# Kernel optimization log

Hardware: AMD Instinct MI355X
Metric: run time of the kernel (lower is better)

## Reference

```python
import jax, jax.numpy as jnp
import numpy as np

ALPHA = 0.2  # LeakyReLU negative slope


def setup_inputs() -> dict:
    key = jax.random.key(0)
    k1, k2, k3, k4 = jax.random.split(key, 4)
    B, N, IN_F, OUT_F = 8, 2048, 128, 64
    inputs = jax.random.normal(k1, (B, N, IN_F), dtype=jnp.float32)
    nodes_embedding = jax.random.normal(k2, (B, N, OUT_F), dtype=jnp.float32)
    # xavier-uniform-like init (gain 1.414)
    limW = 1.414 * np.sqrt(6.0 / (IN_F + OUT_F))
    W = jax.random.uniform(k3, (IN_F, OUT_F), dtype=jnp.float32, minval=-limW, maxval=limW)
    lima = 1.414 * np.sqrt(6.0 / (4 * OUT_F + 1))
    a = jax.random.uniform(k4, (4 * OUT_F, 1), dtype=jnp.float32, minval=-lima, maxval=lima)
    return {"inputs": inputs, "nodes_embedding": nodes_embedding, "W": W, "a": a}


def reference(inputs, nodes_embedding, W, a):
    # x_w: [B,N,F]
    x_w = jnp.matmul(inputs, W)
    # h: [B,N,2F]
    h = jnp.concatenate([nodes_embedding, x_w], axis=2)
    twoF = h.shape[-1]
    # Separable form of concat-based attention: a_input[b,i,j] = [h_i, h_j],
    # so a_input @ a = (h_i . a1) + (h_j . a2). Avoids the O(B*N^2*4F) tensor.
    a1 = a[:twoF, 0]  # [2F]
    a2 = a[twoF:, 0]  # [2F]
    s1 = jnp.einsum('bnf,f->bn', h, a1)  # [B,N]
    s2 = jnp.einsum('bnf,f->bn', h, a2)  # [B,N]
    e = jax.nn.leaky_relu(s1[:, :, None] + s2[:, None, :], negative_slope=ALPHA)  # [B,N,N]
    attention = jax.nn.softmax(e, axis=2)  # softmax over j
    # dropout: eval mode (training=False) -> identity
    h_prime = jnp.matmul(attention, x_w)  # [B,N,F]
    return (jax.nn.relu(h_prime), attention)
```

## Files before the change

kernel.cpp:

```cpp
#include <hip/hip_runtime.h>

#define ALPHA 0.2f
#define B_    8
#define N_    2048
#define INF_  128
#define OUTF_ 64

typedef __attribute__((ext_vector_type(8))) short short8;
typedef __attribute__((ext_vector_type(4))) float f32x4;

__device__ __forceinline__ unsigned short f2bf(float f) {
    unsigned int x = __float_as_uint(f);
    return (unsigned short)((x + 0x7fffu + ((x >> 16) & 1u)) >> 16);
}

__global__ __launch_bounds__(256) void prep_kernel(
    const float* __restrict__ inp,
    const float* __restrict__ nodes,
    const float* __restrict__ Wm,
    const float* __restrict__ av,
    unsigned short* __restrict__ xwT,
    float* __restrict__ s1_out,
    float* __restrict__ s2_out)
{
    __shared__ float w_lds[INF_ * OUTF_];
    __shared__ float in_lds[16 * INF_];
    __shared__ __align__(16) unsigned short t_lds[64 * 16];
    const int tid  = threadIdx.x;
    const int wave = tid >> 6, lane = tid & 63;
    const int r0   = blockIdx.x * 16;

    {
        const float4* Wv = (const float4*)Wm;
        float4* wd = (float4*)w_lds;
        #pragma unroll
        for (int q = 0; q < 8; q++) wd[tid + q * 256] = Wv[tid + q * 256];
        const float4* Iv = (const float4*)(inp + (size_t)r0 * INF_);
        float4* id4 = (float4*)in_lds;
        id4[tid]       = Iv[tid];
        id4[tid + 256] = Iv[tid + 256];
    }
    __syncthreads();

    float acc[4] = {0.f, 0.f, 0.f, 0.f};
    const float* inw = &in_lds[(wave * 4) * INF_];
    #pragma unroll 4
    for (int k = 0; k < INF_; k++) {
        float wv = w_lds[k * OUTF_ + lane];
        acc[0] += inw[k]            * wv;
        acc[1] += inw[INF_ + k]     * wv;
        acc[2] += inw[2 * INF_ + k] * wv;
        acc[3] += inw[3 * INF_ + k] * wv;
    }

    const float a1n = av[lane];
    const float a1x = av[64 + lane];
    const float a2n = av[128 + lane];
    const float a2x = av[192 + lane];

    #pragma unroll
    for (int rr = 0; rr < 4; rr++) {
        const int row = r0 + wave * 4 + rr;
        float nf = nodes[(size_t)row * OUTF_ + lane];
        float p1 = nf * a1n + acc[rr] * a1x;
        float p2 = nf * a2n + acc[rr] * a2x;
        #pragma unroll
        for (int off = 32; off; off >>= 1) {
            p1 += __shfl_down(p1, off);
            p2 += __shfl_down(p2, off);
        }
        if (lane == 0) { s1_out[row] = p1; s2_out[row] = p2; }
        t_lds[lane * 16 + wave * 4 + rr] = f2bf(acc[rr]);
    }
    __syncthreads();

    {
        const int n  = tid >> 2, c0 = (tid & 3) * 4;
        const int b  = r0 >> 11, rb = r0 & (N_ - 1);
        *(uint2*)(xwT + ((size_t)b * OUTF_ + n) * N_ + rb + c0) =
            *(const uint2*)&t_lds[n * 16 + c0];
    }
}

__global__ __launch_bounds__(256) void attn_kernel(
    const unsigned short* __restrict__ xwT,
    const float* __restrict__ s1g,
    const float* __restrict__ s2g,
    float* __restrict__ out_h,
    float* __restrict__ out_att)
{
    __shared__ float s2_lds[N_];
    __shared__ float s1_lds[64];
    __shared__ float m_lds[64];
    __shared__ float li_lds[64];
    __shared__ float redmax[4];

    const int tid  = threadIdx.x;
    const int wave = tid >> 6, lane = tid & 63;
    const int b  = blockIdx.x >> 5;
    const int i0 = (blockIdx.x & 31) << 6;

    {
        const float4* s2v = (const float4*)(s2g + b * N_);
        float4* d4 = (float4*)s2_lds;
        d4[tid]       = s2v[tid];
        d4[tid + 256] = s2v[tid + 256];
    }
    if (tid < 64) s1_lds[tid] = s1g[b * N_ + i0 + tid];
    __syncthreads();

    {
        float lm = -1e30f;
        for (int idx = tid; idx < N_; idx += 256) lm = fmaxf(lm, s2_lds[idx]);
        #pragma unroll
        for (int off = 32; off; off >>= 1) lm = fmaxf(lm, __shfl_xor(lm, off));
        if (lane == 0) redmax[wave] = lm;
    }
    __syncthreads();
    const float s2max = fmaxf(fmaxf(redmax[0], redmax[1]),
                              fmaxf(redmax[2], redmax[3]));

    {
        const int i = tid >> 2, jo = tid & 3;
        const float s1v = s1_lds[i];
        const float vm = s1v + s2max;
        const float m = vm > 0.f ? vm : ALPHA * vm;
        float l = 0.f;
        for (int j4 = jo * 4; j4 < N_; j4 += 16) {
            float4 s = *(const float4*)&s2_lds[j4];
            float v0 = s1v + s.x, v1 = s1v + s.y, v2 = s1v + s.z, v3 = s1v + s.w;
            l += __expf(fmaxf(v0, ALPHA * v0) - m);
            l += __expf(fmaxf(v1, ALPHA * v1) - m);
            l += __expf(fmaxf(v2, ALPHA * v2) - m);
            l += __expf(fmaxf(v3, ALPHA * v3) - m);
        }
        l += __shfl_xor(l, 1);
        l += __shfl_xor(l, 2);
        if (jo == 0) { m_lds[i] = m; li_lds[i] = 1.f / l; }
    }
    __syncthreads();

    const int row16 = lane & 15;
    const int quad  = lane >> 4;
    const int irow  = wave * 16 + row16;
    const float s1v = s1_lds[irow];
    const float mr  = m_lds[irow];
    const float lir = li_lds[irow];

    const unsigned short* bptr[4];
    #pragma unroll
    for (int g = 0; g < 4; g++)
        bptr[g] = xwT + ((size_t)b * OUTF_ + g * 16 + row16) * N_ + quad * 8;

    float* attp = out_att + ((size_t)(b * N_ + i0 + irow)) * N_ + quad * 8;
    const float* s2q = s2_lds + quad * 8;

    f32x4 acc0 = {0.f,0.f,0.f,0.f}, acc1 = {0.f,0.f,0.f,0.f};
    f32x4 acc2 = {0.f,0.f,0.f,0.f}, acc3 = {0.f,0.f,0.f,0.f};

    uint4 bnext[4];
    #pragma unroll
    for (int g = 0; g < 4; g++) bnext[g] = *(const uint4*)bptr[g];

    for (int jt = 0; jt < N_; jt += 32) {
        uint4 bc0 = bnext[0], bc1 = bnext[1], bc2 = bnext[2], bc3 = bnext[3];
        const int jn = (jt + 32) & (N_ - 1);
        #pragma unroll
        for (int g = 0; g < 4; g++) bnext[g] = *(const uint4*)(bptr[g] + jn);

        float4 sa = *(const float4*)(s2q + jt);
        float4 sb = *(const float4*)(s2q + jt + 4);
        float av8[8];
        {
            float v;
            v = s1v + sa.x; av8[0] = __expf(fmaxf(v, ALPHA * v) - mr) * lir;
            v = s1v + sa.y; av8[1] = __expf(fmaxf(v, ALPHA * v) - mr) * lir;
            v = s1v + sa.z; av8[2] = __expf(fmaxf(v, ALPHA * v) - mr) * lir;
            v = s1v + sa.w; av8[3] = __expf(fmaxf(v, ALPHA * v) - mr) * lir;
            v = s1v + sb.x; av8[4] = __expf(fmaxf(v, ALPHA * v) - mr) * lir;
            v = s1v + sb.y; av8[5] = __expf(fmaxf(v, ALPHA * v) - mr) * lir;
            v = s1v + sb.z; av8[6] = __expf(fmaxf(v, ALPHA * v) - mr) * lir;
            v = s1v + sb.w; av8[7] = __expf(fmaxf(v, ALPHA * v) - mr) * lir;
        }
        *(float4*)(attp + jt)     = make_float4(av8[0], av8[1], av8[2], av8[3]);
        *(float4*)(attp + jt + 4) = make_float4(av8[4], av8[5], av8[6], av8[7]);

        short8 a8;
        #pragma unroll
        for (int jj = 0; jj < 8; jj++) a8[jj] = (short)f2bf(av8[jj]);

        acc0 = __builtin_amdgcn_mfma_f32_16x16x32_bf16(a8, *(short8*)&bc0, acc0, 0, 0, 0);
        acc1 = __builtin_amdgcn_mfma_f32_16x16x32_bf16(a8, *(short8*)&bc1, acc1, 0, 0, 0);
        acc2 = __builtin_amdgcn_mfma_f32_16x16x32_bf16(a8, *(short8*)&bc2, acc2, 0, 0, 0);
        acc3 = __builtin_amdgcn_mfma_f32_16x16x32_bf16(a8, *(short8*)&bc3, acc3, 0, 0, 0);
    }

    {
        const size_t hb = ((size_t)(b * N_) + i0 + wave * 16) * OUTF_;
        #pragma unroll
        for (int r = 0; r < 4; r++) {
            const size_t ro = hb + (size_t)(quad * 4 + r) * OUTF_ + row16;
            out_h[ro]      = fmaxf(acc0[r], 0.f);
            out_h[ro + 16] = fmaxf(acc1[r], 0.f);
            out_h[ro + 32] = fmaxf(acc2[r], 0.f);
            out_h[ro + 48] = fmaxf(acc3[r], 0.f);
        }
    }
}

extern "C" void kernel_launch(void* const* d_in, const int* in_sizes, int n_in,
                              void* d_out, int out_size, void* d_ws, size_t ws_size,
                              hipStream_t stream) {
    const float* inp   = (const float*)d_in[0];
    const float* nodes = (const float*)d_in[1];
    const float* Wm    = (const float*)d_in[2];
    const float* av    = (const float*)d_in[3];

    float* out_h   = (float*)d_out;
    float* out_att = out_h + (size_t)B_ * N_ * OUTF_;

    unsigned short* xwT = (unsigned short*)d_ws;
    float* s1_ws = (float*)((char*)d_ws + (size_t)B_ * OUTF_ * N_ * sizeof(unsigned short));
    float* s2_ws = s1_ws + (size_t)B_ * N_;

    prep_kernel<<<(B_ * N_) / 16, 256, 0, stream>>>(inp, nodes, Wm, av,
                                                    xwT, s1_ws, s2_ws);
    attn_kernel<<<(B_ * N_) / 64, 256, 0, stream>>>(xwT, s1_ws, s2_ws,
                                                    out_h, out_att);
}
```

Baseline: 193.1 us.

## Split attention kernel over key dimension with LDS cross-wave reduction

Result: no change. 193.8 us (+0.3%).

```diff
diff --git a/kernel.cpp b/kernel.cpp
--- a/kernel.cpp
+++ b/kernel.cpp
@@ -82,7 +82,7 @@
     }
 }
 
-__global__ __launch_bounds__(256) void attn_kernel(
+__global__ __launch_bounds__(256, 4) void attn_kernel(
     const unsigned short* __restrict__ xwT,
     const float* __restrict__ s1g,
     const float* __restrict__ s2g,
@@ -90,15 +90,16 @@
     float* __restrict__ out_att)
 {
     __shared__ float s2_lds[N_];
-    __shared__ float s1_lds[64];
-    __shared__ float m_lds[64];
-    __shared__ float li_lds[64];
+    __shared__ float s1_lds[16];
+    __shared__ float m_lds[16];
+    __shared__ float li_lds[16];
     __shared__ float redmax[4];
+    __shared__ __align__(16) float red_lds[4][16][68];
 
     const int tid  = threadIdx.x;
     const int wave = tid >> 6, lane = tid & 63;
-    const int b  = blockIdx.x >> 5;
-    const int i0 = (blockIdx.x & 31) << 6;
+    const int b   = blockIdx.x >> 7;
+    const int i0g = blockIdx.x * 16;
 
     {
         const float4* s2v = (const float4*)(s2g + b * N_);
@@ -106,7 +107,7 @@
         d4[tid]       = s2v[tid];
         d4[tid + 256] = s2v[tid + 256];
     }
-    if (tid < 64) s1_lds[tid] = s1g[b * N_ + i0 + tid];
+    if (tid < 16) s1_lds[tid] = s1g[i0g + tid];
     __syncthreads();
 
     {
@@ -121,12 +122,12 @@
                               fmaxf(redmax[2], redmax[3]));
 
     {
-        const int i = tid >> 2, jo = tid & 3;
+        const int i = tid >> 4, jo = tid & 15;
         const float s1v = s1_lds[i];
         const float vm = s1v + s2max;
         const float m = vm > 0.f ? vm : ALPHA * vm;
         float l = 0.f;
-        for (int j4 = jo * 4; j4 < N_; j4 += 16) {
+        for (int j4 = jo * 4; j4 < N_; j4 += 64) {
             float4 s = *(const float4*)&s2_lds[j4];
             float v0 = s1v + s.x, v1 = s1v + s.y, v2 = s1v + s.z, v3 = s1v + s.w;
             l += __expf(fmaxf(v0, ALPHA * v0) - m);
@@ -134,26 +135,26 @@
             l += __expf(fmaxf(v2, ALPHA * v2) - m);
             l += __expf(fmaxf(v3, ALPHA * v3) - m);
         }
-        l += __shfl_xor(l, 1);
-        l += __shfl_xor(l, 2);
+        #pragma unroll
+        for (int off = 8; off; off >>= 1) l += __shfl_xor(l, off);
         if (jo == 0) { m_lds[i] = m; li_lds[i] = 1.f / l; }
     }
     __syncthreads();
 
     const int row16 = lane & 15;
     const int quad  = lane >> 4;
-    const int irow  = wave * 16 + row16;
-    const float s1v = s1_lds[irow];
-    const float mr  = m_lds[irow];
-    const float lir = li_lds[irow];
+    const int jbase = wave * 512;
+    const float s1v = s1_lds[row16];
+    const float mr  = m_lds[row16];
+    const float lir = li_lds[row16];
 
     const unsigned short* bptr[4];
     #pragma unroll
     for (int g = 0; g < 4; g++)
-        bptr[g] = xwT + ((size_t)b * OUTF_ + g * 16 + row16) * N_ + quad * 8;
-
-    float* attp = out_att + ((size_t)(b * N_ + i0 + irow)) * N_ + quad * 8;
-    const float* s2q = s2_lds + quad * 8;
+        bptr[g] = xwT + ((size_t)b * OUTF_ + g * 16 + row16) * N_ + jbase + quad * 8;
+
+    float* attp = out_att + (size_t)(i0g + row16) * N_ + jbase + quad * 8;
+    const float* s2q = s2_lds + jbase + quad * 8;
 
     f32x4 acc0 = {0.f,0.f,0.f,0.f}, acc1 = {0.f,0.f,0.f,0.f};
     f32x4 acc2 = {0.f,0.f,0.f,0.f}, acc3 = {0.f,0.f,0.f,0.f};
@@ -162,9 +163,9 @@
     #pragma unroll
     for (int g = 0; g < 4; g++) bnext[g] = *(const uint4*)bptr[g];
 
-    for (int jt = 0; jt < N_; jt += 32) {
+    for (int jt = 0; jt < 512; jt += 32) {
         uint4 bc0 = bnext[0], bc1 = bnext[1], bc2 = bnext[2], bc3 = bnext[3];
-        const int jn = (jt + 32) & (N_ - 1);
+        const int jn = (jt + 32) & 511;
         #pragma unroll
         for (int g = 0; g < 4; g++) bnext[g] = *(const uint4*)(bptr[g] + jn);
 
@@ -182,12 +183,17 @@
             v = s1v + sb.z; av8[6] = __expf(fmaxf(v, ALPHA * v) - mr) * lir;
             v = s1v + sb.w; av8[7] = __expf(fmaxf(v, ALPHA * v) - mr) * lir;
         }
-        *(float4*)(attp + jt)     = make_float4(av8[0], av8[1], av8[2], av8[3]);
-        *(float4*)(attp + jt + 4) = make_float4(av8[4], av8[5], av8[6], av8[7]);
-
-        short8 a8;
-        #pragma unroll
-        for (int jj = 0; jj < 8; jj++) a8[jj] = (short)f2bf(av8[jj]);
+        f32x4 o0 = {av8[0], av8[1], av8[2], av8[3]};
+        f32x4 o1 = {av8[4], av8[5], av8[6], av8[7]};
+        __builtin_nontemporal_store(o0, (f32x4*)(attp + jt));
+        __builtin_nontemporal_store(o1, (f32x4*)(attp + jt + 4));
+
+        uint4 pk;
+        pk.x = __builtin_amdgcn_perm(__float_as_uint(av8[1]), __float_as_uint(av8[0]), 0x07060302u);
+        pk.y = __builtin_amdgcn_perm(__float_as_uint(av8[3]), __float_as_uint(av8[2]), 0x07060302u);
+        pk.z = __builtin_amdgcn_perm(__float_as_uint(av8[5]), __float_as_uint(av8[4]), 0x07060302u);
+        pk.w = __builtin_amdgcn_perm(__float_as_uint(av8[7]), __float_as_uint(av8[6]), 0x07060302u);
+        short8 a8 = *(short8*)&pk;
 
         acc0 = __builtin_amdgcn_mfma_f32_16x16x32_bf16(a8, *(short8*)&bc0, acc0, 0, 0, 0);
         acc1 = __builtin_amdgcn_mfma_f32_16x16x32_bf16(a8, *(short8*)&bc1, acc1, 0, 0, 0);
@@ -195,16 +201,28 @@
         acc3 = __builtin_amdgcn_mfma_f32_16x16x32_bf16(a8, *(short8*)&bc3, acc3, 0, 0, 0);
     }
 
-    {
-        const size_t hb = ((size_t)(b * N_) + i0 + wave * 16) * OUTF_;
-        #pragma unroll
-        for (int r = 0; r < 4; r++) {
-            const size_t ro = hb + (size_t)(quad * 4 + r) * OUTF_ + row16;
-            out_h[ro]      = fmaxf(acc0[r], 0.f);
-            out_h[ro + 16] = fmaxf(acc1[r], 0.f);
-            out_h[ro + 32] = fmaxf(acc2[r], 0.f);
-            out_h[ro + 48] = fmaxf(acc3[r], 0.f);
-        }
+    #pragma unroll
+    for (int r = 0; r < 4; r++) {
+        float* rw = &red_lds[wave][quad * 4 + r][row16];
+        rw[0]  = acc0[r];
+        rw[16] = acc1[r];
+        rw[32] = acc2[r];
+        rw[48] = acc3[r];
+    }
+    __syncthreads();
+
+    {
+        const int row = tid >> 4, c0 = (tid & 15) * 4;
+        float4 s0 = *(const float4*)&red_lds[0][row][c0];
+        float4 s1 = *(const float4*)&red_lds[1][row][c0];
+        float4 s2 = *(const float4*)&red_lds[2][row][c0];
+        float4 s3 = *(const float4*)&red_lds[3][row][c0];
+        float4 o;
+        o.x = fmaxf(s0.x + s1.x + s2.x + s3.x, 0.f);
+        o.y = fmaxf(s0.y + s1.y + s2.y + s3.y, 0.f);
+        o.z = fmaxf(s0.z + s1.z + s2.z + s3.z, 0.f);
+        o.w = fmaxf(s0.w + s1.w + s2.w + s3.w, 0.f);
+        *(float4*)(out_h + (size_t)(i0g + row) * OUTF_ + c0) = o;
     }
 }
 
@@ -225,6 +243,6 @@
 
     prep_kernel<<<(B_ * N_) / 16, 256, 0, stream>>>(inp, nodes, Wm, av,
                                                     xwT, s1_ws, s2_ws);
-    attn_kernel<<<(B_ * N_) / 64, 256, 0, stream>>>(xwT, s1_ws, s2_ws,
+    attn_kernel<<<(B_ * N_) / 16, 256, 0, stream>>>(xwT, s1_ws, s2_ws,
                                                     out_h, out_att);
 }
```
